# Kernel optimization log

Measured on AMD Instinct MI355X. Metric: run time of the kernel, lower is better.

Reference implementation:

```python
import jax, jax.numpy as jnp
import numpy as np
from jax import lax

B, N, T, NX = 4, 512, 24, 8
H = 64
PRED_LEN, NY = 12, 1
E_RAND = 8192
EPS = 1e-5


def setup_inputs() -> dict:
    key = jax.random.key(0)
    ks = jax.random.split(key, 24)
    sc = lambda k, shape: (jax.random.normal(k, shape, jnp.float32) * 0.05)
    x = jax.random.normal(ks[0], (B, N, T, NX), jnp.float32)
    er = jax.random.randint(ks[1], (2, E_RAND), 0, N, dtype=jnp.int32)
    loops = jnp.stack([jnp.arange(N, dtype=jnp.int32), jnp.arange(N, dtype=jnp.int32)])
    edge_index = jnp.concatenate([er, loops], axis=1)  # [2, 8704]
    return {
        'x': x,
        'edge_index': edge_index,
        'W_fc': sc(ks[2], (NX, H)), 'b_fc': jnp.zeros((H,), jnp.float32),
        'W1': sc(ks[3], (H, H)), 'a_l1': sc(ks[4], (H,)), 'a_r1': sc(ks[5], (H,)), 'bias1': jnp.zeros((H,), jnp.float32),
        'W2': sc(ks[6], (H, H)), 'a_l2': sc(ks[7], (H,)), 'a_r2': sc(ks[8], (H,)), 'bias2': jnp.zeros((H,), jnp.float32),
        'W_ih': sc(ks[9], (4 * H, H)), 'W_hh': sc(ks[10], (4 * H, H)),
        'b_ih': jnp.zeros((4 * H,), jnp.float32), 'b_hh': jnp.zeros((4 * H,), jnp.float32),
        'g_l': jnp.ones((H,), jnp.float32), 'b_l': jnp.zeros((H,), jnp.float32),
        'g_g': jnp.ones((H,), jnp.float32), 'b_g': jnp.zeros((H,), jnp.float32),
        'W_d': sc(ks[11], (H, PRED_LEN * NY)), 'b_d': jnp.zeros((PRED_LEN * NY,), jnp.float32),
    }


def _layer_norm(x, g, b):
    mu = jnp.mean(x, axis=-1, keepdims=True)
    var = jnp.mean(jnp.square(x - mu), axis=-1, keepdims=True)
    return (x - mu) * lax.rsqrt(var + EPS) * g + b


def _gat(x, W, a_l, a_r, bias, mask):
    # x: [B,N,T,F] -> operate in [B,T,N,H] layout (torch transpose(1,2))
    h = jnp.einsum('bntf,fh->btnh', x, W)          # [B,T,N,H]
    el = jnp.einsum('btnh,h->btn', h, a_l)          # attn_l
    er = jnp.einsum('btnh,h->btn', h, a_r)          # attn_r
    e = el[..., :, None] + er[..., None, :]         # [B,T,N,N]
    e = jax.nn.leaky_relu(e, negative_slope=0.2)
    e = jnp.where(mask, e, -jnp.inf)
    alpha = jax.nn.softmax(e, axis=-1)
    out = jnp.einsum('btmn,btnh->bmth', alpha, h) + bias  # back to [B,N,T,H]
    return jax.nn.gelu(out, approximate=False)


def _lstm(xseq, W_ih, W_hh, b_ih, b_hh):
    # xseq: [M, T, H] -> outputs [M, T, H]; PyTorch gate order i,f,g,o
    M = xseq.shape[0]
    Hh = W_hh.shape[1]
    b = b_ih + b_hh
    def step(carry, xt):
        hprev, cprev = carry
        gates = xt @ W_ih.T + hprev @ W_hh.T + b
        i, f, g, o = jnp.split(gates, 4, axis=-1)
        c = jax.nn.sigmoid(f) * cprev + jax.nn.sigmoid(i) * jnp.tanh(g)
        h = jax.nn.sigmoid(o) * jnp.tanh(c)
        return (h, c), h
    init = (jnp.zeros((M, Hh), xseq.dtype), jnp.zeros((M, Hh), xseq.dtype))
    _, hs = lax.scan(step, init, xseq.transpose(1, 0, 2))  # [T,M,H]
    return hs.transpose(1, 0, 2)


def reference(x, edge_index, W_fc, b_fc, W1, a_l1, a_r1, bias1, W2, a_l2, a_r2, bias2,
              W_ih, W_hh, b_ih, b_hh, g_l, b_l, g_g, b_g, W_d, b_d):
    Bb, Nn, Tt, _ = x.shape
    mask = jnp.zeros((Nn, Nn), bool).at[edge_index[0], edge_index[1]].set(True)
    x_h = jnp.einsum('bntf,fh->bnth', x, W_fc) + b_fc          # fc
    g1 = _gat(x_h, W1, a_l1, a_r1, bias1, mask)                # conv1
    g2 = _gat(g1, W2, a_l2, a_r2, bias2, mask)                 # conv2
    l = _lstm(x_h.reshape(Bb * Nn, Tt, -1), W_ih, W_hh, b_ih, b_hh).reshape(Bb, Nn, Tt, -1)
    h = _layer_norm(g2, g_g, b_g) + _layer_norm(l, g_l, b_l)
    last = h[:, :, -1, :]                                       # [B,N,H]
    out = last @ W_d + b_d                                      # [B,N,pred_len*ny]
    return out.reshape(Bb, Nn, PRED_LEN, NY)
```

## Files before the change

kernel.cpp:

```cpp
#include <hip/hip_runtime.h>
#include <hip/hip_bf16.h>
#include <math.h>

#define BB 4
#define NN 512
#define TT 24
#define NXF 8
#define HH 64
#define PRED 12
#define MM (BB*NN)

typedef __attribute__((ext_vector_type(8))) short short8;
typedef __attribute__((ext_vector_type(4))) float f32x4;
typedef unsigned short ushort;

#define WS_HBUF    0
#define WS_H2      131072
#define WS_HL      262144
#define WS_EL      393216
#define WS_ER      395264
#define WS_EL2     397312
#define WS_ER2     399360
#define WS_WCOMB   401408
#define WS_BCOMB   403456
#define WS_WHHFRAG 403712

__device__ inline float sigm(float x){ return 1.f/(1.f+__expf(-x)); }
__device__ inline float tanh_fast(float x){ float e=__expf(2.f*x); return 1.f - 2.f/(e+1.f); }
__device__ inline float gelu_exact(float x){ return 0.5f*x*(1.f+erff(x*0.70710678118654752440f)); }
__device__ inline ushort f2bu(float f){
    unsigned b=__float_as_uint(f);
    return (ushort)((b + 0x7FFFu + ((b>>16)&1u))>>16);
}
__device__ inline float bu2f(ushort u){ return __uint_as_float(((unsigned)u)<<16); }

__device__ inline void split8(const float* f, short8& hi, short8& lo){
    #pragma unroll
    for (int j = 0; j < 8; ++j){
        ushort h = f2bu(f[j]);
        hi[j] = (short)h;
        lo[j] = (short)f2bu(f[j] - bu2f(h));
    }
}

__global__ __launch_bounds__(256,2) void gat1pre_kernel(
    const float* __restrict__ x, const float* __restrict__ Wfc, const float* __restrict__ bfc,
    const float* __restrict__ W1, const float* __restrict__ al1, const float* __restrict__ ar1,
    const float* __restrict__ Wih, const float* __restrict__ Whh,
    const float* __restrict__ bih, const float* __restrict__ bhh,
    float* __restrict__ Hbuf, float* __restrict__ el, float* __restrict__ er,
    float* __restrict__ wcombG, float* __restrict__ bcombG,
    ushort* __restrict__ whhfrag)
{
    __shared__ float sw1[HH*HH];
    __shared__ float swfc[NXF*HH];
    __shared__ float sb[HH], sal[HH], sar[HH];
    __shared__ float sxh[4][68];
    __shared__ float sx[4][NXF];
    const int t = threadIdx.x;

    if (blockIdx.x >= 512){
        const int f = blockIdx.x - 512;
        const int ng = t;
        float accf = 0.f, accb = 0.f;
        const float* wr = Wih + ng*64;
        #pragma unroll
        for (int k = 0; k < 64; ++k){
            float wv = wr[k];
            accf += Wfc[f*64 + k] * wv;
            accb += bfc[k] * wv;
        }
        wcombG[f*256 + ng] = accf;
        if (f == 0) bcombG[ng] = accb + bih[ng] + bhh[ng];
        #pragma unroll
        for (int u = 0; u < 8; ++u){
            int o = f*2048 + u*256 + t;
            int F  = o >> 9;
            int ln = (o >> 3) & 63;
            int j  = o & 7;
            int w_ = F >> 3, tt = (F >> 1) & 3, ks = F & 1;
            int q = ln >> 4, c = ln & 15;
            int ngx = (w_ + 4*tt)*16 + c;
            whhfrag[o] = f2bu(Whh[ngx*64 + ks*32 + q*8 + j]);
        }
        return;
    }

    const int r = t >> 6, h = t & 63;
    #pragma unroll
    for (int i = 0; i < 16; ++i) sw1[t + 256*i] = W1[t + 256*i];
    swfc[t] = Wfc[t];
    swfc[t+256] = Wfc[t+256];
    if (t < 64) sb[t] = bfc[t];
    else if (t < 128) sal[t-64] = al1[t-64];
    else if (t < 192) sar[t-128] = ar1[t-128];
    if (t < 32){
        int rr = t >> 3, f = t & 7;
        sx[rr][f] = x[(size_t)(blockIdx.x*4 + rr)*(TT*NXF) + (TT-1)*NXF + f];
    }
    __syncthreads();
    float xh = sb[h];
    #pragma unroll
    for (int f = 0; f < NXF; ++f) xh += sx[r][f]*swfc[f*HH + h];
    sxh[r][h] = xh;
    __syncthreads();
    float acc = 0.f;
    const float4* xr = (const float4*)&sxh[r][0];
    #pragma unroll
    for (int k4 = 0; k4 < 16; ++k4){
        float4 xv = xr[k4];
        acc += xv.x*sw1[(4*k4+0)*HH+h] + xv.y*sw1[(4*k4+1)*HH+h]
             + xv.z*sw1[(4*k4+2)*HH+h] + xv.w*sw1[(4*k4+3)*HH+h];
    }
    const int m = blockIdx.x*4 + r;
    Hbuf[(size_t)m*HH + h] = acc;
    float v1 = acc*sal[h], v2 = acc*sar[h];
    #pragma unroll
    for (int o = 32; o; o >>= 1){ v1 += __shfl_xor(v1,o); v2 += __shfl_xor(v2,o); }
    if (h == 0){ el[m] = v1; er[m] = v2; }
}

#define LHS 72
#define LXS 40
__global__ __launch_bounds__(256,2) void mid_fused_kernel(
    const float* __restrict__ Hbuf, const float* __restrict__ el_in, const float* __restrict__ er_in,
    const int* __restrict__ ei, int E,
    const float* __restrict__ bias1,
    const float* __restrict__ W2, const float* __restrict__ al2, const float* __restrict__ ar2,
    float* __restrict__ H2, float* __restrict__ el2, float* __restrict__ er2,
    const float* __restrict__ x,
    const float* __restrict__ wcombG, const float* __restrict__ bcombG,
    const ushort* __restrict__ whhfrag,
    float* __restrict__ hl)
{
    __shared__ __align__(16) char smem[58880];
    const int t = threadIdx.x;
    const int lane = t & 63;
    const int w = t >> 6;
    const int quad = lane >> 4;
    const int c16 = lane & 15;

    if (blockIdx.x >= 128){
        ushort* hbi = (ushort*)smem;
        ushort* hlo = (ushort*)(smem + 4608);
        ushort* xls = (ushort*)(smem + 9216);
        const int m0 = (blockIdx.x - 128) * 16;

        {
            unsigned* h0 = (unsigned*)hbi;
            unsigned* l0 = (unsigned*)hlo;
            for (int i = t; i < 2*16*LHS/2; i += 256){ h0[i] = 0u; l0[i] = 0u; }
            unsigned* xw = (unsigned*)xls;
            for (int i = t; i < TT*16*LXS/2; i += 256) xw[i] = 0u;
        }
        short8 bw[4][2]; short8 bx[4]; float bc[4];
        #pragma unroll
        for (int tt = 0; tt < 4; ++tt){
            const int ng = (w + 4*tt)*16 + c16;
            bc[tt] = bcombG[ng];
            #pragma unroll
            for (int ks = 0; ks < 2; ++ks)
                bw[tt][ks] = *(const short8*)&whhfrag[(((w*4+tt)*2)+ks)*512 + lane*8];
            short8 vx = {0,0,0,0,0,0,0,0};
            if (quad == 0){
                #pragma unroll
                for (int j = 0; j < 8; ++j) vx[j] = (short)f2bu(wcombG[j*256 + ng]);
            }
            bx[tt] = vx;
        }
        __syncthreads();
        for (int i = t; i < 16*TT*NXF; i += 256){
            int r = i / (TT*NXF);
            int rem = i - r*(TT*NXF);
            int st = rem >> 3, f = rem & 7;
            xls[st*(16*LXS) + r*LXS + f] = f2bu(x[(size_t)(m0+r)*(TT*NXF) + rem]);
        }
        __syncthreads();

        float cst[4] = {0,0,0,0};
        float hf[4]  = {0,0,0,0};

        for (int st = 0; st < TT; ++st){
            const int p = st & 1;
            const ushort* hb  = hbi + p*(16*LHS);
            const ushort* hl_ = hlo + p*(16*LHS);
            short8 ahi0 = *(const short8*)&hb[c16*LHS + quad*8];
            short8 ahi1 = *(const short8*)&hb[c16*LHS + 32 + quad*8];
            short8 alo0 = *(const short8*)&hl_[c16*LHS + quad*8];
            short8 alo1 = *(const short8*)&hl_[c16*LHS + 32 + quad*8];
            short8 ax   = *(const short8*)&xls[st*(16*LXS) + c16*LXS + quad*8];
            f32x4 acc[4];
            #pragma unroll
            for (int tt = 0; tt < 4; ++tt){
                f32x4 a = {bc[tt], bc[tt], bc[tt], bc[tt]};
                a = __builtin_amdgcn_mfma_f32_16x16x32_bf16(ax,   bx[tt],    a, 0,0,0);
                a = __builtin_amdgcn_mfma_f32_16x16x32_bf16(ahi0, bw[tt][0], a, 0,0,0);
                a = __builtin_amdgcn_mfma_f32_16x16x32_bf16(ahi1, bw[tt][1], a, 0,0,0);
                a = __builtin_amdgcn_mfma_f32_16x16x32_bf16(alo0, bw[tt][0], a, 0,0,0);
                a = __builtin_amdgcn_mfma_f32_16x16x32_bf16(alo1, bw[tt][1], a, 0,0,0);
                acc[tt] = a;
            }
            ushort* ho   = hbi + (p^1)*(16*LHS);
            ushort* lo_o = hlo + (p^1)*(16*LHS);
            #pragma unroll
            for (int reg = 0; reg < 4; ++reg){
                float gi = acc[0][reg], gf = acc[1][reg], gg = acc[2][reg], go = acc[3][reg];
                float cn = sigm(gf)*cst[reg] + sigm(gi)*tanh_fast(gg);
                cst[reg] = cn;
                float hn = sigm(go)*tanh_fast(cn);
                hf[reg] = hn;
                ushort hu = f2bu(hn);
                float lov = hn - bu2f(hu);
                int addr = (quad*4+reg)*LHS + w*16 + c16;
                ho[addr] = hu;
                lo_o[addr] = f2bu(lov);
            }
            __syncthreads();
        }
        #pragma unroll
        for (int reg = 0; reg < 4; ++reg)
            hl[(size_t)(m0 + quad*4 + reg)*HH + w*16 + c16] = hf[reg];
        return;
    }

    unsigned (*smask)[16] = (unsigned(*)[16])smem;
    float* er_s  = (float*)(smem + 1024);
    float* sal   = (float*)(smem + 3072);
    float* sar   = (float*)(smem + 3328);
    float (*alpha)[516] = (float(*)[516])(smem + 3584);
    float* uSpace = (float*)(smem + 36608);
    float (*xh2)[68] = (float(*)[68])(smem + 54528);

    const int b = blockIdx.x >> 5;
    const int m0 = (blockIdx.x & 31) * 16;
    const int l = lane;
    float (*HT)[70] = (float(*)[70])uSpace;

    if (t < 64) sal[t] = al2[t]; else if (t < 128) sar[t-64] = ar2[t-64];
    ((unsigned*)smask)[t] = 0;
    er_s[t] = er_in[b*NN + t];
    er_s[t+256] = er_in[b*NN + t + 256];
    __syncthreads();
    for (int e = t; e < E; e += 256){
        int s = ei[e];
        unsigned rl = (unsigned)(s - m0);
        if (rl < 16u){
            int d = ei[E + e];
            atomicOr(&smask[rl][d>>5], 1u << (d & 31));
        }
    }
    const float* Hbase = Hbuf + (size_t)b*NN*HH;
    const int nn = t >> 2, cc = t & 3;
    float4 r0,r1,r2,r3;
    {
        const float4* src = (const float4*)(Hbase + (size_t)nn*HH + cc*16);
        r0 = src[0]; r1 = src[1]; r2 = src[2]; r3 = src[3];
    }
    __syncthreads();
    for (int q = 0; q < 4; ++q){
        const int i = w*4 + q;
        const float elv = el_in[b*NN + m0 + i];
        float e8[8]; unsigned mk = 0; float mx = -1e30f;
        #pragma unroll
        for (int j = 0; j < 8; ++j){
            int n = l + 64*j;
            float ev = elv + er_s[n];
            ev = ev >= 0.f ? ev : 0.2f*ev;
            unsigned mb = (smask[i][(l>>5) + 2*j] >> (l & 31)) & 1u;
            e8[j] = ev;
            if (mb){ mk |= (1u<<j); mx = fmaxf(mx, ev); }
        }
        #pragma unroll
        for (int o = 32; o; o >>= 1) mx = fmaxf(mx, __shfl_xor(mx, o));
        float s = 0.f;
        #pragma unroll
        for (int j = 0; j < 8; ++j){
            float p = ((mk>>j) & 1u) ? __expf(e8[j]-mx) : 0.f;
            e8[j] = p; s += p;
        }
        #pragma unroll
        for (int o = 32; o; o >>= 1) s += __shfl_xor(s, o);
        const float inv = 1.f/s;
        #pragma unroll
        for (int j = 0; j < 8; ++j) alpha[i][l + 64*j] = e8[j]*inv;
    }
    __syncthreads();

    f32x4 acc = {0.f,0.f,0.f,0.f};
    for (int tile = 0; tile < 8; ++tile){
        {
            float v[16] = {r0.x,r0.y,r0.z,r0.w, r1.x,r1.y,r1.z,r1.w,
                           r2.x,r2.y,r2.z,r2.w, r3.x,r3.y,r3.z,r3.w};
            #pragma unroll
            for (int jj = 0; jj < 16; ++jj) HT[cc*16 + jj][nn] = v[jj];
        }
        if (tile < 7){
            const float4* src = (const float4*)(Hbase + (size_t)((tile+1)*64 + nn)*HH + cc*16);
            r0 = src[0]; r1 = src[1]; r2 = src[2]; r3 = src[3];
        }
        __syncthreads();
        #pragma unroll
        for (int ks = 0; ks < 2; ++ks){
            const int k0 = tile*64 + ks*32;
            const float* ap = &alpha[c16][k0 + quad*8];
            float4 a0 = *(const float4*)ap;
            float4 a1 = *(const float4*)(ap + 4);
            const float* bp = &HT[w*16 + c16][ks*32 + quad*8];
            float2 b0 = *(const float2*)bp,     b1 = *(const float2*)(bp+2);
            float2 b2 = *(const float2*)(bp+4), b3 = *(const float2*)(bp+6);
            float af[8] = {a0.x,a0.y,a0.z,a0.w,a1.x,a1.y,a1.z,a1.w};
            float bf[8] = {b0.x,b0.y,b1.x,b1.y,b2.x,b2.y,b3.x,b3.y};
            short8 ahi, alo, bhi, blo;
            split8(af, ahi, alo);
            split8(bf, bhi, blo);
            acc = __builtin_amdgcn_mfma_f32_16x16x32_bf16(ahi, bhi, acc, 0,0,0);
            acc = __builtin_amdgcn_mfma_f32_16x16x32_bf16(alo, bhi, acc, 0,0,0);
            acc = __builtin_amdgcn_mfma_f32_16x16x32_bf16(ahi, blo, acc, 0,0,0);
        }
        __syncthreads();
    }
    {
        const int h = w*16 + c16;
        const float bv = bias1[h];
        #pragma unroll
        for (int reg = 0; reg < 4; ++reg)
            xh2[quad*4 + reg][h] = gelu_exact(acc[reg] + bv);
    }
    __syncthreads();
    float* sw2 = uSpace;
    #pragma unroll
    for (int i = 0; i < 16; ++i) sw2[t + 256*i] = W2[t + 256*i];
    __syncthreads();
    {
        const int h = l;
        for (int q = 0; q < 4; ++q){
            const int i = w + 4*q;
            float acc2 = 0.f;
            const float4* xr = (const float4*)&xh2[i][0];
            #pragma unroll
            for (int k4 = 0; k4 < 16; ++k4){
                float4 xv = xr[k4];
                acc2 += xv.x*sw2[(4*k4+0)*HH+h] + xv.y*sw2[(4*k4+1)*HH+h]
                      + xv.z*sw2[(4*k4+2)*HH+h] + xv.w*sw2[(4*k4+3)*HH+h];
            }
            const int m = b*NN + m0 + i;
            H2[(size_t)m*HH + h] = acc2;
            float v1 = acc2*sal[h], v2 = acc2*sar[h];
            #pragma unroll
            for (int o = 32; o; o >>= 1){ v1 += __shfl_xor(v1,o); v2 += __shfl_xor(v2,o); }
            if (h == 0){ el2[m] = v1; er2[m] = v2; }
        }
    }
}

__global__ __launch_bounds__(256,2) void attn2_final_kernel(
    const float* __restrict__ Hbuf, const float* __restrict__ el_in, const float* __restrict__ er_in,
    const int* __restrict__ ei, int E,
    const float* __restrict__ bias2,
    const float* __restrict__ hl,
    const float* __restrict__ g_l, const float* __restrict__ b_l,
    const float* __restrict__ g_g, const float* __restrict__ b_g,
    const float* __restrict__ W_d, const float* __restrict__ b_d,
    float* __restrict__ out)
{
    __shared__ __align__(16) char smem[54016];
    unsigned (*smask)[16] = (unsigned(*)[16])smem;
    float* er_s  = (float*)(smem + 1024);
    float (*alpha)[516] = (float(*)[516])(smem + 3072);
    float* uSpace = (float*)(smem + 36096);

    const int t = threadIdx.x;
    const int b = blockIdx.x >> 5;
    const int m0 = (blockIdx.x & 31) * 16;
    const int l = t & 63, w = t >> 6;
    const int quad = l >> 4, c16 = l & 15;
    float (*HT)[70] = (float(*)[70])uSpace;

    ((unsigned*)smask)[t] = 0;
    er_s[t] = er_in[b*NN + t];
    er_s[t+256] = er_in[b*NN + t + 256];
    __syncthreads();
    for (int e = t; e < E; e += 256){
        int s = ei[e];
        unsigned rl = (unsigned)(s - m0);
        if (rl < 16u){
            int d = ei[E + e];
            atomicOr(&smask[rl][d>>5], 1u << (d & 31));
        }
    }
    const float* Hbase = Hbuf + (size_t)b*NN*HH;
    const int nn = t >> 2, cc = t & 3;
    float4 r0,r1,r2,r3;
    {
        const float4* src = (const float4*)(Hbase + (size_t)nn*HH + cc*16);
        r0 = src[0]; r1 = src[1]; r2 = src[2]; r3 = src[3];
    }
    __syncthreads();
    for (int q = 0; q < 4; ++q){
        const int i = w*4 + q;
        const float elv = el_in[b*NN + m0 + i];
        float e8[8]; unsigned mk = 0; float mx = -1e30f;
        #pragma unroll
        for (int j = 0; j < 8; ++j){
            int n = l + 64*j;
            float ev = elv + er_s[n];
            ev = ev >= 0.f ? ev : 0.2f*ev;
            unsigned mb = (smask[i][(l>>5) + 2*j] >> (l & 31)) & 1u;
            e8[j] = ev;
            if (mb){ mk |= (1u<<j); mx = fmaxf(mx, ev); }
        }
        #pragma unroll
        for (int o = 32; o; o >>= 1) mx = fmaxf(mx, __shfl_xor(mx, o));
        float s = 0.f;
        #pragma unroll
        for (int j = 0; j < 8; ++j){
            float p = ((mk>>j) & 1u) ? __expf(e8[j]-mx) : 0.f;
            e8[j] = p; s += p;
        }
        #pragma unroll
        for (int o = 32; o; o >>= 1) s += __shfl_xor(s, o);
        const float inv = 1.f/s;
        #pragma unroll
        for (int j = 0; j < 8; ++j) alpha[i][l + 64*j] = e8[j]*inv;
    }
    __syncthreads();

    f32x4 acc = {0.f,0.f,0.f,0.f};
    for (int tile = 0; tile < 8; ++tile){
        {
            float v[16] = {r0.x,r0.y,r0.z,r0.w, r1.x,r1.y,r1.z,r1.w,
                           r2.x,r2.y,r2.z,r2.w, r3.x,r3.y,r3.z,r3.w};
            #pragma unroll
            for (int jj = 0; jj < 16; ++jj) HT[cc*16 + jj][nn] = v[jj];
        }
        if (tile < 7){
            const float4* src = (const float4*)(Hbase + (size_t)((tile+1)*64 + nn)*HH + cc*16);
            r0 = src[0]; r1 = src[1]; r2 = src[2]; r3 = src[3];
        }
        __syncthreads();
        #pragma unroll
        for (int ks = 0; ks < 2; ++ks){
            const int k0 = tile*64 + ks*32;
            const float* ap = &alpha[c16][k0 + quad*8];
            float4 a0 = *(const float4*)ap;
            float4 a1 = *(const float4*)(ap + 4);
            const float* bp = &HT[w*16 + c16][ks*32 + quad*8];
            float2 b0 = *(const float2*)bp,     b1 = *(const float2*)(bp+2);
            float2 b2 = *(const float2*)(bp+4), b3 = *(const float2*)(bp+6);
            float af[8] = {a0.x,a0.y,a0.z,a0.w,a1.x,a1.y,a1.z,a1.w};
            float bf[8] = {b0.x,b0.y,b1.x,b1.y,b2.x,b2.y,b3.x,b3.y};
            short8 ahi, alo, bhi, blo;
            split8(af, ahi, alo);
            split8(bf, bhi, blo);
            acc = __builtin_amdgcn_mfma_f32_16x16x32_bf16(ahi, bhi, acc, 0,0,0);
            acc = __builtin_amdgcn_mfma_f32_16x16x32_bf16(alo, bhi, acc, 0,0,0);
            acc = __builtin_amdgcn_mfma_f32_16x16x32_bf16(ahi, blo, acc, 0,0,0);
        }
        __syncthreads();
    }
    float* sg2  = (float*)(smem + 3072);
    float* sdec = (float*)(smem + 36096);
    {
        const int h = w*16 + c16;
        const float bv = bias2[h];
        #pragma unroll
        for (int reg = 0; reg < 4; ++reg)
            sg2[(quad*4 + reg)*HH + h] = gelu_exact(acc[reg] + bv);
    }
    __syncthreads();
    const int gbase = b*NN + m0;
    {
        const int h = l;
        for (int q = 0; q < 4; ++q){
            const int ml = w*4 + q;
            float gv = sg2[ml*HH + h];
            float lv = hl[(size_t)(gbase + ml)*HH + h];

            float s1 = gv;
            #pragma unroll
            for (int o = 32; o; o >>= 1) s1 += __shfl_xor(s1, o);
            float dg = gv - s1*(1.f/64.f);
            float v1 = dg*dg;
            #pragma unroll
            for (int o = 32; o; o >>= 1) v1 += __shfl_xor(v1, o);
            float lng = dg*rsqrtf(v1*(1.f/64.f) + 1e-5f)*g_g[h] + b_g[h];

            float s2 = lv;
            #pragma unroll
            for (int o = 32; o; o >>= 1) s2 += __shfl_xor(s2, o);
            float dl = lv - s2*(1.f/64.f);
            float v2 = dl*dl;
            #pragma unroll
            for (int o = 32; o; o >>= 1) v2 += __shfl_xor(v2, o);
            float lnl = dl*rsqrtf(v2*(1.f/64.f) + 1e-5f)*g_l[h] + b_l[h];

            sdec[ml*HH + h] = lng + lnl;
        }
    }
    __syncthreads();
    if (t < 16*PRED){
        int rr = t / PRED, pp = t - rr*PRED;
        float a = b_d[pp];
        #pragma unroll
        for (int k = 0; k < HH; ++k) a += sdec[rr*HH + k]*W_d[k*PRED + pp];
        out[(size_t)(gbase + rr)*PRED + pp] = a;
    }
}

extern "C" void kernel_launch(void* const* d_in, const int* in_sizes, int n_in,
                              void* d_out, int out_size, void* d_ws, size_t ws_size,
                              hipStream_t stream){
    const float* x    = (const float*)d_in[0];
    const int*   ei   = (const int*)  d_in[1];
    const float* Wfc  = (const float*)d_in[2];
    const float* bfc  = (const float*)d_in[3];
    const float* W1   = (const float*)d_in[4];
    const float* al1  = (const float*)d_in[5];
    const float* ar1  = (const float*)d_in[6];
    const float* bias1= (const float*)d_in[7];
    const float* W2   = (const float*)d_in[8];
    const float* al2  = (const float*)d_in[9];
    const float* ar2  = (const float*)d_in[10];
    const float* bias2= (const float*)d_in[11];
    const float* Wih  = (const float*)d_in[12];
    const float* Whh  = (const float*)d_in[13];
    const float* bih  = (const float*)d_in[14];
    const float* bhh  = (const float*)d_in[15];
    const float* g_l  = (const float*)d_in[16];
    const float* b_l  = (const float*)d_in[17];
    const float* g_g  = (const float*)d_in[18];
    const float* b_g  = (const float*)d_in[19];
    const float* W_d  = (const float*)d_in[20];
    const float* b_d  = (const float*)d_in[21];

    float* ws = (float*)d_ws;
    const int E = in_sizes[1] / 2;

    gat1pre_kernel<<<512 + 8, 256, 0, stream>>>(x, Wfc, bfc, W1, al1, ar1,
                                                Wih, Whh, bih, bhh,
                                                ws+WS_HBUF, ws+WS_EL, ws+WS_ER,
                                                ws+WS_WCOMB, ws+WS_BCOMB,
                                                (ushort*)(ws+WS_WHHFRAG));
    mid_fused_kernel<<<256, 256, 0, stream>>>(ws+WS_HBUF, ws+WS_EL, ws+WS_ER,
                                              ei, E, bias1, W2, al2, ar2,
                                              ws+WS_H2, ws+WS_EL2, ws+WS_ER2,
                                              x, ws+WS_WCOMB, ws+WS_BCOMB,
                                              (const ushort*)(ws+WS_WHHFRAG),
                                              ws+WS_HL);
    attn2_final_kernel<<<BB*(NN/16), 256, 0, stream>>>(ws+WS_H2, ws+WS_EL2, ws+WS_ER2,
                                                       ei, E, bias2,
                                                       ws+WS_HL,
                                                       g_l, b_l, g_g, b_g, W_d, b_d,
                                                       (float*)d_out);
}
```

Before: 150.7 us.

## Store GAT node features pre-split into transposed bf16 hi/lo for direct MFMA loads

```diff
diff --git a/kernel.cpp b/kernel.cpp
--- a/kernel.cpp
+++ b/kernel.cpp
@@ -14,8 +14,10 @@
 typedef __attribute__((ext_vector_type(4))) float f32x4;
 typedef unsigned short ushort;
 
-#define WS_HBUF    0
-#define WS_H2      131072
+#define WS_H1THI   0
+#define WS_H1TLO   65536
+#define WS_H2THI   131072
+#define WS_H2TLO   196608
 #define WS_HL      262144
 #define WS_EL      393216
 #define WS_ER      395264
@@ -25,6 +27,9 @@
 #define WS_BCOMB   403456
 #define WS_WHHFRAG 403712
 
+#define LHS 72
+#define LXS 40
+
 __device__ inline float sigm(float x){ return 1.f/(1.f+__expf(-x)); }
 __device__ inline float tanh_fast(float x){ float e=__expf(2.f*x); return 1.f - 2.f/(e+1.f); }
 __device__ inline float gelu_exact(float x){ return 0.5f*x*(1.f+erff(x*0.70710678118654752440f)); }
@@ -48,7 +53,8 @@
     const float* __restrict__ W1, const float* __restrict__ al1, const float* __restrict__ ar1,
     const float* __restrict__ Wih, const float* __restrict__ Whh,
     const float* __restrict__ bih, const float* __restrict__ bhh,
-    float* __restrict__ Hbuf, float* __restrict__ el, float* __restrict__ er,
+    ushort* __restrict__ H1Thi, ushort* __restrict__ H1Tlo,
+    float* __restrict__ el, float* __restrict__ er,
     float* __restrict__ wcombG, float* __restrict__ bcombG,
     ushort* __restrict__ whhfrag)
 {
@@ -113,21 +119,26 @@
              + xv.z*sw1[(4*k4+2)*HH+h] + xv.w*sw1[(4*k4+3)*HH+h];
     }
     const int m = blockIdx.x*4 + r;
-    Hbuf[(size_t)m*HH + h] = acc;
+    {
+        int bb = m >> 9, ml = m & 511;
+        ushort hu = f2bu(acc);
+        H1Thi[((size_t)(bb*HH + h))*NN + ml] = hu;
+        H1Tlo[((size_t)(bb*HH + h))*NN + ml] = f2bu(acc - bu2f(hu));
+    }
     float v1 = acc*sal[h], v2 = acc*sar[h];
     #pragma unroll
     for (int o = 32; o; o >>= 1){ v1 += __shfl_xor(v1,o); v2 += __shfl_xor(v2,o); }
     if (h == 0){ el[m] = v1; er[m] = v2; }
 }
 
-#define LHS 72
-#define LXS 40
 __global__ __launch_bounds__(256,2) void mid_fused_kernel(
-    const float* __restrict__ Hbuf, const float* __restrict__ el_in, const float* __restrict__ er_in,
+    const ushort* __restrict__ H1Thi, const ushort* __restrict__ H1Tlo,
+    const float* __restrict__ el_in, const float* __restrict__ er_in,
     const int* __restrict__ ei, int E,
     const float* __restrict__ bias1,
     const float* __restrict__ W2, const float* __restrict__ al2, const float* __restrict__ ar2,
-    float* __restrict__ H2, float* __restrict__ el2, float* __restrict__ er2,
+    ushort* __restrict__ H2Thi, ushort* __restrict__ H2Tlo,
+    float* __restrict__ el2, float* __restrict__ er2,
     const float* __restrict__ x,
     const float* __restrict__ wcombG, const float* __restrict__ bcombG,
     const ushort* __restrict__ whhfrag,
@@ -234,7 +245,6 @@
     const int b = blockIdx.x >> 5;
     const int m0 = (blockIdx.x & 31) * 16;
     const int l = lane;
-    float (*HT)[70] = (float(*)[70])uSpace;
 
     if (t < 64) sal[t] = al2[t]; else if (t < 128) sar[t-64] = ar2[t-64];
     ((unsigned*)smask)[t] = 0;
@@ -248,13 +258,6 @@
             int d = ei[E + e];
             atomicOr(&smask[rl][d>>5], 1u << (d & 31));
         }
-    }
-    const float* Hbase = Hbuf + (size_t)b*NN*HH;
-    const int nn = t >> 2, cc = t & 3;
-    float4 r0,r1,r2,r3;
-    {
-        const float4* src = (const float4*)(Hbase + (size_t)nn*HH + cc*16);
-        r0 = src[0]; r1 = src[1]; r2 = src[2]; r3 = src[3];
     }
     __syncthreads();
     for (int q = 0; q < 4; ++q){
@@ -286,39 +289,23 @@
     }
     __syncthreads();
 
+    const ushort* bhp = H1Thi + ((size_t)(b*HH + w*16 + c16))*NN;
+    const ushort* blp = H1Tlo + ((size_t)(b*HH + w*16 + c16))*NN;
     f32x4 acc = {0.f,0.f,0.f,0.f};
-    for (int tile = 0; tile < 8; ++tile){
-        {
-            float v[16] = {r0.x,r0.y,r0.z,r0.w, r1.x,r1.y,r1.z,r1.w,
-                           r2.x,r2.y,r2.z,r2.w, r3.x,r3.y,r3.z,r3.w};
-            #pragma unroll
-            for (int jj = 0; jj < 16; ++jj) HT[cc*16 + jj][nn] = v[jj];
-        }
-        if (tile < 7){
-            const float4* src = (const float4*)(Hbase + (size_t)((tile+1)*64 + nn)*HH + cc*16);
-            r0 = src[0]; r1 = src[1]; r2 = src[2]; r3 = src[3];
-        }
-        __syncthreads();
-        #pragma unroll
-        for (int ks = 0; ks < 2; ++ks){
-            const int k0 = tile*64 + ks*32;
-            const float* ap = &alpha[c16][k0 + quad*8];
-            float4 a0 = *(const float4*)ap;
-            float4 a1 = *(const float4*)(ap + 4);
-            const float* bp = &HT[w*16 + c16][ks*32 + quad*8];
-            float2 b0 = *(const float2*)bp,     b1 = *(const float2*)(bp+2);
-            float2 b2 = *(const float2*)(bp+4), b3 = *(const float2*)(bp+6);
-            float af[8] = {a0.x,a0.y,a0.z,a0.w,a1.x,a1.y,a1.z,a1.w};
-            float bf[8] = {b0.x,b0.y,b1.x,b1.y,b2.x,b2.y,b3.x,b3.y};
-            short8 ahi, alo, bhi, blo;
-            split8(af, ahi, alo);
-            split8(bf, bhi, blo);
-            acc = __builtin_amdgcn_mfma_f32_16x16x32_bf16(ahi, bhi, acc, 0,0,0);
-            acc = __builtin_amdgcn_mfma_f32_16x16x32_bf16(alo, bhi, acc, 0,0,0);
-            acc = __builtin_amdgcn_mfma_f32_16x16x32_bf16(ahi, blo, acc, 0,0,0);
-        }
-        __syncthreads();
-    }
+    for (int k0 = 0; k0 < NN; k0 += 32){
+        const float* ap = &alpha[c16][k0 + quad*8];
+        float4 a0 = *(const float4*)ap;
+        float4 a1 = *(const float4*)(ap + 4);
+        float af[8] = {a0.x,a0.y,a0.z,a0.w,a1.x,a1.y,a1.z,a1.w};
+        short8 a_h, a_l;
+        split8(af, a_h, a_l);
+        short8 b_h = *(const short8*)&bhp[k0 + quad*8];
+        short8 b_l = *(const short8*)&blp[k0 + quad*8];
+        acc = __builtin_amdgcn_mfma_f32_16x16x32_bf16(a_h, b_h, acc, 0,0,0);
+        acc = __builtin_amdgcn_mfma_f32_16x16x32_bf16(a_l, b_h, acc, 0,0,0);
+        acc = __builtin_amdgcn_mfma_f32_16x16x32_bf16(a_h, b_l, acc, 0,0,0);
+    }
+    __syncthreads();
     {
         const int h = w*16 + c16;
         const float bv = bias1[h];
@@ -326,7 +313,6 @@
         for (int reg = 0; reg < 4; ++reg)
             xh2[quad*4 + reg][h] = gelu_exact(acc[reg] + bv);
     }
-    __syncthreads();
     float* sw2 = uSpace;
     #pragma unroll
     for (int i = 0; i < 16; ++i) sw2[t + 256*i] = W2[t + 256*i];
@@ -344,7 +330,9 @@
                       + xv.z*sw2[(4*k4+2)*HH+h] + xv.w*sw2[(4*k4+3)*HH+h];
             }
             const int m = b*NN + m0 + i;
-            H2[(size_t)m*HH + h] = acc2;
+            ushort hu = f2bu(acc2);
+            H2Thi[((size_t)(b*HH + h))*NN + (m0 + i)] = hu;
+            H2Tlo[((size_t)(b*HH + h))*NN + (m0 + i)] = f2bu(acc2 - bu2f(hu));
             float v1 = acc2*sal[h], v2 = acc2*sar[h];
             #pragma unroll
             for (int o = 32; o; o >>= 1){ v1 += __shfl_xor(v1,o); v2 += __shfl_xor(v2,o); }
@@ -354,7 +342,8 @@
 }
 
 __global__ __launch_bounds__(256,2) void attn2_final_kernel(
-    const float* __restrict__ Hbuf, const float* __restrict__ el_in, const float* __restrict__ er_in,
+    const ushort* __restrict__ H2Thi, const ushort* __restrict__ H2Tlo,
+    const float* __restrict__ el_in, const float* __restrict__ er_in,
     const int* __restrict__ ei, int E,
     const float* __restrict__ bias2,
     const float* __restrict__ hl,
@@ -367,14 +356,12 @@
     unsigned (*smask)[16] = (unsigned(*)[16])smem;
     float* er_s  = (float*)(smem + 1024);
     float (*alpha)[516] = (float(*)[516])(smem + 3072);
-    float* uSpace = (float*)(smem + 36096);
 
     const int t = threadIdx.x;
     const int b = blockIdx.x >> 5;
     const int m0 = (blockIdx.x & 31) * 16;
     const int l = t & 63, w = t >> 6;
     const int quad = l >> 4, c16 = l & 15;
-    float (*HT)[70] = (float(*)[70])uSpace;
 
     ((unsigned*)smask)[t] = 0;
     er_s[t] = er_in[b*NN + t];
@@ -387,13 +374,6 @@
             int d = ei[E + e];
             atomicOr(&smask[rl][d>>5], 1u << (d & 31));
         }
-    }
-    const float* Hbase = Hbuf + (size_t)b*NN*HH;
-    const int nn = t >> 2, cc = t & 3;
-    float4 r0,r1,r2,r3;
-    {
-        const float4* src = (const float4*)(Hbase + (size_t)nn*HH + cc*16);
-        r0 = src[0]; r1 = src[1]; r2 = src[2]; r3 = src[3];
     }
     __syncthreads();
     for (int q = 0; q < 4; ++q){
@@ -425,39 +405,23 @@
     }
     __syncthreads();
 
+    const ushort* bhp = H2Thi + ((size_t)(b*HH + w*16 + c16))*NN;
+    const ushort* blp = H2Tlo + ((size_t)(b*HH + w*16 + c16))*NN;
     f32x4 acc = {0.f,0.f,0.f,0.f};
-    for (int tile = 0; tile < 8; ++tile){
-        {
-            float v[16] = {r0.x,r0.y,r0.z,r0.w, r1.x,r1.y,r1.z,r1.w,
-                           r2.x,r2.y,r2.z,r2.w, r3.x,r3.y,r3.z,r3.w};
-            #pragma unroll
-            for (int jj = 0; jj < 16; ++jj) HT[cc*16 + jj][nn] = v[jj];
-        }
-        if (tile < 7){
-            const float4* src = (const float4*)(Hbase + (size_t)((tile+1)*64 + nn)*HH + cc*16);
-            r0 = src[0]; r1 = src[1]; r2 = src[2]; r3 = src[3];
-        }
-        __syncthreads();
-        #pragma unroll
-        for (int ks = 0; ks < 2; ++ks){
-            const int k0 = tile*64 + ks*32;
-            const float* ap = &alpha[c16][k0 + quad*8];
-            float4 a0 = *(const float4*)ap;
-            float4 a1 = *(const float4*)(ap + 4);
-            const float* bp = &HT[w*16 + c16][ks*32 + quad*8];
-            float2 b0 = *(const float2*)bp,     b1 = *(const float2*)(bp+2);
-            float2 b2 = *(const float2*)(bp+4), b3 = *(const float2*)(bp+6);
-            float af[8] = {a0.x,a0.y,a0.z,a0.w,a1.x,a1.y,a1.z,a1.w};
-            float bf[8] = {b0.x,b0.y,b1.x,b1.y,b2.x,b2.y,b3.x,b3.y};
-            short8 ahi, alo, bhi, blo;
-            split8(af, ahi, alo);
-            split8(bf, bhi, blo);
-            acc = __builtin_amdgcn_mfma_f32_16x16x32_bf16(ahi, bhi, acc, 0,0,0);
-            acc = __builtin_amdgcn_mfma_f32_16x16x32_bf16(alo, bhi, acc, 0,0,0);
-            acc = __builtin_amdgcn_mfma_f32_16x16x32_bf16(ahi, blo, acc, 0,0,0);
-        }
-        __syncthreads();
-    }
+    for (int k0 = 0; k0 < NN; k0 += 32){
+        const float* ap = &alpha[c16][k0 + quad*8];
+        float4 a0 = *(const float4*)ap;
+        float4 a1 = *(const float4*)(ap + 4);
+        float af[8] = {a0.x,a0.y,a0.z,a0.w,a1.x,a1.y,a1.z,a1.w};
+        short8 a_h, a_l;
+        split8(af, a_h, a_l);
+        short8 b_h = *(const short8*)&bhp[k0 + quad*8];
+        short8 b_l = *(const short8*)&blp[k0 + quad*8];
+        acc = __builtin_amdgcn_mfma_f32_16x16x32_bf16(a_h, b_h, acc, 0,0,0);
+        acc = __builtin_amdgcn_mfma_f32_16x16x32_bf16(a_l, b_h, acc, 0,0,0);
+        acc = __builtin_amdgcn_mfma_f32_16x16x32_bf16(a_h, b_l, acc, 0,0,0);
+    }
+    __syncthreads();
     float* sg2  = (float*)(smem + 3072);
     float* sdec = (float*)(smem + 36096);
     {
@@ -538,16 +502,20 @@
 
     gat1pre_kernel<<<512 + 8, 256, 0, stream>>>(x, Wfc, bfc, W1, al1, ar1,
                                                 Wih, Whh, bih, bhh,
-                                                ws+WS_HBUF, ws+WS_EL, ws+WS_ER,
+                                                (ushort*)(ws+WS_H1THI), (ushort*)(ws+WS_H1TLO),
+                                                ws+WS_EL, ws+WS_ER,
                                                 ws+WS_WCOMB, ws+WS_BCOMB,
                                                 (ushort*)(ws+WS_WHHFRAG));
-    mid_fused_kernel<<<256, 256, 0, stream>>>(ws+WS_HBUF, ws+WS_EL, ws+WS_ER,
+    mid_fused_kernel<<<256, 256, 0, stream>>>((const ushort*)(ws+WS_H1THI), (const ushort*)(ws+WS_H1TLO),
+                                              ws+WS_EL, ws+WS_ER,
                                               ei, E, bias1, W2, al2, ar2,
-                                              ws+WS_H2, ws+WS_EL2, ws+WS_ER2,
+                                              (ushort*)(ws+WS_H2THI), (ushort*)(ws+WS_H2TLO),
+                                              ws+WS_EL2, ws+WS_ER2,
                                               x, ws+WS_WCOMB, ws+WS_BCOMB,
                                               (const ushort*)(ws+WS_WHHFRAG),
                                               ws+WS_HL);
-    attn2_final_kernel<<<BB*(NN/16), 256, 0, stream>>>(ws+WS_H2, ws+WS_EL2, ws+WS_ER2,
+    attn2_final_kernel<<<BB*(NN/16), 256, 0, stream>>>((const ushort*)(ws+WS_H2THI), (const ushort*)(ws+WS_H2TLO),
+                                                       ws+WS_EL2, ws+WS_ER2,
                                                        ei, E, bias2,
                                                        ws+WS_HL,
                                                        g_l, b_l, g_g, b_g, W_d, b_d,
```

Measured after the change: 151.2 us. About the same (+0.3%).
